# Kernel tuning notes

Measured on AMD Instinct MI355X. Metric: run time of the kernel, lower is better.

The kernel has to match this reference:

```python
import jax, jax.numpy as jnp
import numpy as np
import math

B, S, HID = 2, 2048, 2048
H, HKV, D, L = 16, 4, 128, 64
THETA = 10000.0
N_REP = H // HKV


def _rope(t, pos, theta=THETA):
    # t: [B, h, S, D], pos: [B, S] int
    d = t.shape[-1]
    inv_freq = 1.0 / (theta ** (jnp.arange(0, d, 2, dtype=jnp.float32) / d))  # [d/2]
    ang = pos.astype(jnp.float32)[:, :, None] * inv_freq  # [B, S, d/2]
    cos = jnp.concatenate([jnp.cos(ang), jnp.cos(ang)], axis=-1)[:, None]  # [B,1,S,d]
    sin = jnp.concatenate([jnp.sin(ang), jnp.sin(ang)], axis=-1)[:, None]
    t1, t2 = t[..., : d // 2], t[..., d // 2 :]
    rot = jnp.concatenate([-t2, t1], axis=-1)
    return t * cos + rot * sin


def setup_inputs() -> dict:
    key = jax.random.key(0)
    ks = jax.random.split(key, 9)
    sc = lambda fin: 1.0 / math.sqrt(fin)
    x = jax.random.normal(ks[0], (B, S, HID), dtype=jnp.float32)
    position_ids = jnp.broadcast_to(jnp.arange(S, dtype=jnp.int32), (B, S))
    # additive causal mask [1,1,S,S]
    causal = jnp.triu(jnp.full((S, S), -1e9, dtype=jnp.float32), k=1)
    attention_mask = causal[None, None]
    Wq = jax.random.normal(ks[1], (HID, H * D), dtype=jnp.float32) * sc(HID)
    Wk = jax.random.normal(ks[2], (HID, HKV * D), dtype=jnp.float32) * sc(HID)
    Wv = jax.random.normal(ks[3], (HID, HKV * D), dtype=jnp.float32) * sc(HID)
    Wql = jax.random.normal(ks[4], (D, L), dtype=jnp.float32) * sc(D)
    Wkl = jax.random.normal(ks[5], (D, L), dtype=jnp.float32) * sc(D)
    Wvl = jax.random.normal(ks[6], (D, L), dtype=jnp.float32) * sc(D)
    Wo = jax.random.normal(ks[7], (H * D, HID), dtype=jnp.float32) * sc(H * D)
    return {"x": x, "position_ids": position_ids, "attention_mask": attention_mask,
            "Wq": Wq, "Wk": Wk, "Wv": Wv, "Wql": Wql, "Wkl": Wkl, "Wvl": Wvl, "Wo": Wo}


def reference(x, position_ids, attention_mask, Wq, Wk, Wv, Wql, Wkl, Wvl, Wo):
    b, s, _ = x.shape
    q = (x @ Wq).reshape(b, s, H, D).transpose(0, 2, 1, 3)    # [B,H,S,D]
    k = (x @ Wk).reshape(b, s, HKV, D).transpose(0, 2, 1, 3)  # [B,HKV,S,D]
    v = (x @ Wv).reshape(b, s, HKV, D).transpose(0, 2, 1, 3)
    q = _rope(q, position_ids)
    k = _rope(k, position_ids)
    # latent compression per head-dim
    q_l = jnp.einsum('bhsd,dl->bhsl', q, Wql)  # [B,H,S,L]
    k_l = jnp.einsum('bhsd,dl->bhsl', k, Wkl)  # [B,HKV,S,L]
    v_l = jnp.einsum('bhsd,dl->bhsl', v, Wvl)
    k_l = jnp.repeat(k_l, N_REP, axis=1)  # repeat_kv -> [B,H,S,L]
    v_l = jnp.repeat(v_l, N_REP, axis=1)
    scale = math.sqrt(L)
    attn = jnp.einsum('bhql,bhkl->bhqk', q_l, k_l) / scale
    attn = attn + attention_mask
    attn = jax.nn.softmax(attn, axis=-1)
    out = jnp.einsum('bhqk,bhkl->bhql', attn, v_l)  # [B,H,S,L]
    if L < D:
        out = jnp.pad(out, ((0, 0), (0, 0), (0, 0), (0, D - L)))
    out = out.transpose(0, 2, 1, 3).reshape(b, s, H * D)
    return out @ Wo
```

## Files before the change

### kernel.cpp

```cpp
#include <hip/hip_runtime.h>
#include <cstddef>

constexpr int kB   = 2;
constexpr int kS   = 2048;
constexpr int kHID = 2048;
constexpr int kH   = 16;
constexpr int kHKV = 4;
constexpr int kD   = 128;
constexpr int kL   = 64;
constexpr int kTok = kB * kS;
constexpr int kNQKV = kH * kD + 2 * kHKV * kD;

typedef __attribute__((ext_vector_type(8))) short bf16x8;
typedef __attribute__((ext_vector_type(4))) float f32x4;

static __device__ __forceinline__ short f2bf(float f) {
  union { float f; unsigned u; } v{f};
  const unsigned r = (v.u + 0x7fff + ((v.u >> 16) & 1)) >> 16;
  return (short)r;
}
static __device__ __forceinline__ float bf2f(short s) {
  union { unsigned u; float f; } v;
  v.u = ((unsigned)(unsigned short)s) << 16;
  return v.f;
}

static __device__ __forceinline__ bf16x8 pack8(float4 a, float4 b) {
  bf16x8 r;
  r[0] = f2bf(a.x); r[1] = f2bf(a.y); r[2] = f2bf(a.z); r[3] = f2bf(a.w);
  r[4] = f2bf(b.x); r[5] = f2bf(b.y); r[6] = f2bf(b.z); r[7] = f2bf(b.w);
  return r;
}

static __device__ __forceinline__ unsigned cvt_pk_bf16(float lo, float hi) {
  unsigned r;
  asm("v_cvt_pk_bf16_f32 %0, %1, %2" : "=v"(r) : "v"(lo), "v"(hi));
  return r;
}

typedef __attribute__((address_space(3))) void       lds_void;
typedef __attribute__((address_space(1))) const void gm_void;
static __device__ __forceinline__ void gload16(const void* g, void* l) {
  __builtin_amdgcn_global_load_lds((gm_void*)g, (lds_void*)l, 16, 0, 0);
}

static __device__ __forceinline__ int2 xcd_swz(int nx, int ny) {
  int wg = blockIdx.y * nx + blockIdx.x;
  const int cpx = (nx * ny) >> 3;
  wg = (wg & 7) * cpx + (wg >> 3);
  int2 r; r.x = wg % nx; r.y = wg / nx;
  return r;
}

__global__ __launch_bounds__(256) void prep_all(
    const float* __restrict__ x, const int* __restrict__ pos,
    const float* __restrict__ Wq, const float* __restrict__ Wk,
    const float* __restrict__ Wv, const float* __restrict__ Wo,
    const float* __restrict__ Wql, const float* __restrict__ Wkl,
    const float* __restrict__ Wvl, short* __restrict__ x_bf,
    float* __restrict__ tbl, short* __restrict__ Wqkv,
    short* __restrict__ WoT, short* __restrict__ WqlT,
    short* __restrict__ WklT, short* __restrict__ WvlT) {
  __shared__ float T[64][65];
  const int bidg = blockIdx.x;
  const int tid = threadIdx.x;

  if (bidg < 4096) {
    const int i = bidg * 256 + tid;
    const float4 a = *(const float4*)&x[(size_t)i * 8];
    const float4 b = *(const float4*)&x[(size_t)i * 8 + 4];
    *(bf16x8*)&x_bf[(size_t)i * 8] = pack8(a, b);
    return;
  }
  if (bidg < 5120) {
    const int idx = (bidg - 4096) * 256 + tid;
    const int i = idx & 63, t = idx >> 6;
    const float p = (float)pos[t];
    const float inv_freq = expf(-(float)i * (9.210340371976184f / 64.0f));
    const float ang = p * inv_freq;
    tbl[t * 128 + i]      = cosf(ang);
    tbl[t * 128 + 64 + i] = sinf(ang);
    return;
  }
  const int rr = tid >> 4, cc = tid & 15;
  if (bidg < 6656) {
    const int idx = bidg - 5120;
    const int n0 = (idx % 48) * 64, k0 = (idx / 48) * 64;
    const float* in; int Nin, nl0;
    if (n0 < 2048)      { in = Wq; Nin = 2048; nl0 = n0; }
    else if (n0 < 2560) { in = Wk; Nin = 512;  nl0 = n0 - 2048; }
    else                { in = Wv; Nin = 512;  nl0 = n0 - 2560; }
#pragma unroll
    for (int ii = 0; ii < 4; ++ii) {
      const int kr = rr + ii * 16;
      const float4 v = *(const float4*)&in[(size_t)(k0 + kr) * Nin + nl0 + cc * 4];
      T[kr][cc * 4 + 0] = v.x; T[kr][cc * 4 + 1] = v.y;
      T[kr][cc * 4 + 2] = v.z; T[kr][cc * 4 + 3] = v.w;
    }
    __syncthreads();
#pragma unroll
    for (int ii = 0; ii < 4; ++ii) {
      const int n = rr + ii * 16;
      const short4 s4 = make_short4(f2bf(T[cc*4+0][n]), f2bf(T[cc*4+1][n]),
                                    f2bf(T[cc*4+2][n]), f2bf(T[cc*4+3][n]));
      *(short4*)&Wqkv[(size_t)(n0 + n) * kHID + k0 + cc * 4] = s4;
    }
    return;
  }
  if (bidg < 7168) {
    const int idx = bidg - 6656;
    const int n0 = (idx % 32) * 64, k0 = (idx / 32) * 64;
#pragma unroll
    for (int ii = 0; ii < 4; ++ii) {
      const int kr = rr + ii * 16;
      const int gr = (((k0 + kr) >> 6) << 7) + ((k0 + kr) & 63);
      const float4 v = *(const float4*)&Wo[(size_t)gr * kHID + n0 + cc * 4];
      T[kr][cc * 4 + 0] = v.x; T[kr][cc * 4 + 1] = v.y;
      T[kr][cc * 4 + 2] = v.z; T[kr][cc * 4 + 3] = v.w;
    }
    __syncthreads();
#pragma unroll
    for (int ii = 0; ii < 4; ++ii) {
      const int n = rr + ii * 16;
      const short4 s4 = make_short4(f2bf(T[cc*4+0][n]), f2bf(T[cc*4+1][n]),
                                    f2bf(T[cc*4+2][n]), f2bf(T[cc*4+3][n]));
      *(short4*)&WoT[(size_t)(n0 + n) * (kH * kL) + k0 + cc * 4] = s4;
    }
    return;
  }
  {
    const int idx = bidg - 7168;
    const int k0 = (idx & 1) * 64;
    const int z = idx >> 1;
    const float* in; short* out; float scale;
    if (z == 0)      { in = Wql; out = WqlT; scale = 0.125f; }
    else if (z == 1) { in = Wkl; out = WklT; scale = 1.0f; }
    else             { in = Wvl; out = WvlT; scale = 1.0f; }
#pragma unroll
    for (int ii = 0; ii < 4; ++ii) {
      const int kr = rr + ii * 16;
      const float4 v = *(const float4*)&in[(size_t)(k0 + kr) * kL + cc * 4];
      T[kr][cc * 4 + 0] = v.x * scale; T[kr][cc * 4 + 1] = v.y * scale;
      T[kr][cc * 4 + 2] = v.z * scale; T[kr][cc * 4 + 3] = v.w * scale;
    }
    __syncthreads();
#pragma unroll
    for (int ii = 0; ii < 4; ++ii) {
      const int n = rr + ii * 16;
      const short4 s4 = make_short4(f2bf(T[cc*4+0][n]), f2bf(T[cc*4+1][n]),
                                    f2bf(T[cc*4+2][n]), f2bf(T[cc*4+3][n]));
      *(short4*)&out[(size_t)n * kD + k0 + cc * 4] = s4;
    }
  }
}

__global__ __launch_bounds__(512) void gemm_qkv8(
    const short* __restrict__ A, const short* __restrict__ Bt,
    short* __restrict__ C0, short* __restrict__ C1, short* __restrict__ C2,
    int K) {
  __shared__ short As[2][256 * 64];
  __shared__ short Bs[2][256 * 64];
  const int tid = threadIdx.x;
  const int lane = tid & 63, w = tid >> 6;
  const int lr = lane & 15, lk = lane >> 4;
  const int wm = w >> 2, wn = w & 3;
  const int2 sw = xcd_swz(kNQKV / 256, kTok / 256);
  const int row0 = sw.y * 256, col0 = sw.x * 256;
  const int NT = K >> 6;

  auto stage = [&](int kt) {
    const int b = kt & 1;
    const int k0 = kt << 6;
#pragma unroll
    for (int j = 0; j < 4; ++j) {
      const int idx = j * 512 + tid;
      const int row = idx >> 3, blk = idx & 7;
      const int gcol = k0 + ((blk ^ (row & 7)) << 3);
      gload16(A + (size_t)(row0 + row) * K + gcol, &As[b][row * 64 + blk * 8]);
    }
#pragma unroll
    for (int j = 0; j < 4; ++j) {
      const int idx = j * 512 + tid;
      const int row = idx >> 3, blk = idx & 7;
      const int gcol = k0 + ((blk ^ (row & 7)) << 3);
      gload16(Bt + (size_t)(col0 + row) * K + gcol, &Bs[b][row * 64 + blk * 8]);
    }
  };

  f32x4 acc[8][4] = {};

  stage(0);
  for (int t = 0; t < NT; ++t) {
    const int b = t & 1;
    if (t + 1 < NT) {
      stage(t + 1);
      asm volatile("s_waitcnt vmcnt(8)" ::: "memory");
    } else {
      asm volatile("s_waitcnt vmcnt(0)" ::: "memory");
    }
    __builtin_amdgcn_s_barrier();

    bf16x8 bb[4][2];
#pragma unroll
    for (int n = 0; n < 4; ++n) {
      const int row = wn * 64 + n * 16 + lr;
#pragma unroll
      for (int ch = 0; ch < 2; ++ch) {
        const int blk = (ch * 4 + lk) ^ (row & 7);
        bb[n][ch] = *(const bf16x8*)&Bs[b][row * 64 + blk * 8];
      }
    }
#pragma unroll
    for (int qm = 0; qm < 2; ++qm) {
      bf16x8 a[4][2];
#pragma unroll
      for (int j = 0; j < 4; ++j) {
        const int row = wm * 128 + (qm * 4 + j) * 16 + lr;
#pragma unroll
        for (int ch = 0; ch < 2; ++ch) {
          const int blk = (ch * 4 + lk) ^ (row & 7);
          a[j][ch] = *(const bf16x8*)&As[b][row * 64 + blk * 8];
        }
      }
      __builtin_amdgcn_s_setprio(1);
#pragma unroll
      for (int j = 0; j < 4; ++j)
#pragma unroll
        for (int n = 0; n < 4; ++n)
#pragma unroll
          for (int ch = 0; ch < 2; ++ch)
            acc[qm * 4 + j][n] = __builtin_amdgcn_mfma_f32_16x16x32_bf16(
                a[j][ch], bb[n][ch], acc[qm * 4 + j][n], 0, 0, 0);
      __builtin_amdgcn_s_setprio(0);
    }
    __builtin_amdgcn_s_barrier();
  }

  short* dst; int ld, cb;
  if (col0 < 2048)      { dst = C0; ld = 2048; cb = col0; }
  else if (col0 < 2560) { dst = C1; ld = 512;  cb = col0 - 2048; }
  else                  { dst = C2; ld = 512;  cb = col0 - 2560; }
  const int crow0 = row0 + wm * 128 + lk * 4;
  const int ccol0 = cb + wn * 64 + lr;
#pragma unroll
  for (int mf = 0; mf < 8; ++mf)
#pragma unroll
    for (int nf = 0; nf < 4; ++nf)
#pragma unroll
      for (int r = 0; r < 4; ++r)
        dst[(size_t)(crow0 + mf * 16 + r) * ld + ccol0 + nf * 16] =
            f2bf(acc[mf][nf][r]);
}

__global__ __launch_bounds__(512) void gemm_out8(
    const short* __restrict__ A, const short* __restrict__ Bt,
    float* __restrict__ C, int M, int N, int K) {
  __shared__ short As[2][256 * 64];
  __shared__ short Bs[2][128 * 64];
  const int tid = threadIdx.x;
  const int lane = tid & 63, w = tid >> 6;
  const int lr = lane & 15, lk = lane >> 4;
  const int wm = w >> 2, wn = w & 3;
  const int2 sw = xcd_swz(N / 128, M / 256);
  const int row0 = sw.y * 256, col0 = sw.x * 128;
  const int NT = K >> 6;

  auto stage = [&](int kt) {
    const int b = kt & 1;
    const int k0 = kt << 6;
#pragma unroll
    for (int j = 0; j < 4; ++j) {
      const int idx = j * 512 + tid;
      const int row = idx >> 3, blk = idx & 7;
      const int gcol = k0 + ((blk ^ (row & 7)) << 3);
      gload16(A + (size_t)(row0 + row) * K + gcol, &As[b][row * 64 + blk * 8]);
    }
#pragma unroll
    for (int j = 0; j < 2; ++j) {
      const int idx = j * 512 + tid;
      const int row = idx >> 3, blk = idx & 7;
      const int gcol = k0 + ((blk ^ (row & 7)) << 3);
      gload16(Bt + (size_t)(col0 + row) * K + gcol, &Bs[b][row * 64 + blk * 8]);
    }
  };

  f32x4 acc[8][2] = {};

  stage(0);
  for (int t = 0; t < NT; ++t) {
    const int b = t & 1;
    if (t + 1 < NT) {
      stage(t + 1);
      asm volatile("s_waitcnt vmcnt(6)" ::: "memory");
    } else {
      asm volatile("s_waitcnt vmcnt(0)" ::: "memory");
    }
    __builtin_amdgcn_s_barrier();

    bf16x8 bb[2][2];
#pragma unroll
    for (int n = 0; n < 2; ++n) {
      const int row = wn * 32 + n * 16 + lr;
#pragma unroll
      for (int ch = 0; ch < 2; ++ch) {
        const int blk = (ch * 4 + lk) ^ (row & 7);
        bb[n][ch] = *(const bf16x8*)&Bs[b][row * 64 + blk * 8];
      }
    }
#pragma unroll
    for (int qm = 0; qm < 2; ++qm) {
      bf16x8 a[4][2];
#pragma unroll
      for (int j = 0; j < 4; ++j) {
        const int row = wm * 128 + (qm * 4 + j) * 16 + lr;
#pragma unroll
        for (int ch = 0; ch < 2; ++ch) {
          const int blk = (ch * 4 + lk) ^ (row & 7);
          a[j][ch] = *(const bf16x8*)&As[b][row * 64 + blk * 8];
        }
      }
      __builtin_amdgcn_s_setprio(1);
#pragma unroll
      for (int j = 0; j < 4; ++j)
#pragma unroll
        for (int n = 0; n < 2; ++n)
#pragma unroll
          for (int ch = 0; ch < 2; ++ch)
            acc[qm * 4 + j][n] = __builtin_amdgcn_mfma_f32_16x16x32_bf16(
                a[j][ch], bb[n][ch], acc[qm * 4 + j][n], 0, 0, 0);
      __builtin_amdgcn_s_setprio(0);
    }
    __builtin_amdgcn_s_barrier();
  }

  const int crow0 = row0 + wm * 128 + lk * 4;
  const int ccol0 = col0 + wn * 32 + lr;
#pragma unroll
  for (int mf = 0; mf < 8; ++mf)
#pragma unroll
    for (int nf = 0; nf < 2; ++nf)
#pragma unroll
      for (int r = 0; r < 4; ++r)
        C[(size_t)(crow0 + mf * 16 + r) * N + ccol0 + nf * 16] = acc[mf][nf][r];
}

__global__ __launch_bounds__(256) void rope_latent_all(
    const short* __restrict__ qb, const short* __restrict__ kb,
    const short* __restrict__ vb, const short* __restrict__ WqlT,
    const short* __restrict__ WklT, const short* __restrict__ WvlT,
    const float* __restrict__ tbl, short* __restrict__ q_l,
    short* __restrict__ k_l, short* __restrict__ v_lT) {
  __shared__ short Tw[4][1280];
  const int yz = blockIdx.y;
  const short* in; const short* WT; short* out; int nh; bool ROPE, TR;
  int bh;
  if (yz < 32)      { in = qb; WT = WqlT; out = q_l;  nh = kH;   ROPE = true;  TR = false; bh = yz; }
  else if (yz < 40) { in = kb; WT = WklT; out = k_l;  nh = kHKV; ROPE = true;  TR = false; bh = yz - 32; }
  else              { in = vb; WT = WvlT; out = v_lT; nh = kHKV; ROPE = false; TR = true;  bh = yz - 40; }

  const int tid = threadIdx.x;
  const int lane = tid & 63;
  const int w = tid >> 6;
  const int lr = lane & 15;
  const int lk = lane >> 4;
  const int b = bh / nh, h = bh % nh;
  const int s0 = blockIdx.x * 64;
  const int srow = s0 + w * 16 + lr;
  const int tok = b * kS + srow;

  const short* ip = in + ((size_t)tok * nh + h) * kD + lk * 8;
  bf16x8 raw[4];
#pragma unroll
  for (int ch = 0; ch < 4; ++ch) raw[ch] = *(const bf16x8*)(ip + ch * 32);

  bf16x8 af[4];
  if (ROPE) {
    float a[4][8];
#pragma unroll
    for (int ch = 0; ch < 4; ++ch)
#pragma unroll
      for (int i = 0; i < 8; ++i) a[ch][i] = bf2f(raw[ch][i]);
    const float* tb = tbl + (size_t)tok * 128;
    float c[2][8], sn[2][8];
#pragma unroll
    for (int g = 0; g < 2; ++g) {
      const float4 cA = *(const float4*)(tb + g * 32 + lk * 8);
      const float4 cB = *(const float4*)(tb + g * 32 + lk * 8 + 4);
      const float4 sA = *(const float4*)(tb + 64 + g * 32 + lk * 8);
      const float4 sB = *(const float4*)(tb + 64 + g * 32 + lk * 8 + 4);
      c[g][0] = cA.x; c[g][1] = cA.y; c[g][2] = cA.z; c[g][3] = cA.w;
      c[g][4] = cB.x; c[g][5] = cB.y; c[g][6] = cB.z; c[g][7] = cB.w;
      sn[g][0] = sA.x; sn[g][1] = sA.y; sn[g][2] = sA.z; sn[g][3] = sA.w;
      sn[g][4] = sB.x; sn[g][5] = sB.y; sn[g][6] = sB.z; sn[g][7] = sB.w;
    }
    float o[4][8];
#pragma unroll
    for (int g = 0; g < 2; ++g)
#pragma unroll
      for (int i = 0; i < 8; ++i) {
        o[g][i]     = a[g][i]     * c[g][i] - a[g + 2][i] * sn[g][i];
        o[g + 2][i] = a[g + 2][i] * c[g][i] + a[g][i]     * sn[g][i];
      }
#pragma unroll
    for (int ch = 0; ch < 4; ++ch)
#pragma unroll
      for (int i = 0; i < 8; ++i) af[ch][i] = f2bf(o[ch][i]);
  } else {
#pragma unroll
    for (int ch = 0; ch < 4; ++ch) af[ch] = raw[ch];
  }

  f32x4 acc[4] = {};
#pragma unroll
  for (int cb = 0; cb < 4; ++cb) {
#pragma unroll
    for (int ch = 0; ch < 4; ++ch) {
      const bf16x8 bfrag =
          *(const bf16x8*)&WT[(size_t)(cb * 16 + lr) * kD + ch * 32 + lk * 8];
      acc[cb] = __builtin_amdgcn_mfma_f32_16x16x32_bf16(af[ch], bfrag,
                                                        acc[cb], 0, 0, 0);
    }
  }

  short* T = Tw[w];
  if (!TR) {
#pragma unroll
    for (int cb = 0; cb < 4; ++cb)
#pragma unroll
      for (int r = 0; r < 4; ++r)
        T[(lk * 4 + r) * 72 + cb * 16 + lr] = f2bf(acc[cb][r]);
    asm volatile("s_waitcnt lgkmcnt(0)" ::: "memory");
#pragma unroll
    for (int it = 0; it < 2; ++it) {
      const int idx = it * 64 + lane;
      const int row = idx >> 3, c8 = (idx & 7) << 3;
      *(bf16x8*)&out[((size_t)bh * kS + s0 + w * 16 + row) * kL + c8] =
          *(const bf16x8*)&T[row * 72 + c8];
    }
  } else {
#pragma unroll
    for (int cb = 0; cb < 4; ++cb)
#pragma unroll
      for (int r = 0; r < 4; ++r)
        T[(cb * 16 + lr) * 20 + lk * 4 + r] = f2bf(acc[cb][r]);
    asm volatile("s_waitcnt lgkmcnt(0)" ::: "memory");
    const size_t orow = ((size_t)bh * kL + lane) * kS + s0 + w * 16;
#pragma unroll
    for (int c = 0; c < 4; ++c)
      *(short4*)&out[orow + c * 4] = *(const short4*)&T[lane * 20 + c * 4];
  }
}

__global__ __launch_bounds__(512) void flash_attn_mfma(
    const short* __restrict__ ql, const short* __restrict__ kl,
    const short* __restrict__ vlT, short* __restrict__ attn_out) {
  constexpr int LDK = 72;
  constexpr int LDV = 136;
  __shared__ short Kt[2][128 * LDK];
  __shared__ short Vt[2][64 * LDV];

  const int tid = threadIdx.x;
  const int lane = tid & 63;
  const int w = tid >> 6;
  const int lr = lane & 15;
  const int lk = lane >> 4;
  const int bid = blockIdx.y;
  const int bx = (bid < 8) ? (2 * bid) : (31 - 2 * bid);
  const int q0 = bx * 128;
  const int bh = blockIdx.x;
  const int b = bh >> 4, h = bh & 15;
  const int hk = h >> 2;
  const int wrow = q0 + w * 16;

  const short* qrow = ql + ((size_t)bh * kS + wrow + lr) * kL;
  bf16x8 qf[2];
  qf[0] = *(const bf16x8*)(qrow + lk * 8);
  qf[1] = *(const bf16x8*)(qrow + 32 + lk * 8);

  f32x4 Of[4] = {};
  float m = -3.0e38f, l = 0.f;

  const short* kgp = kl + (size_t)(b * kHKV + hk) * kS * kL;
  const short* vgp = vlT + (size_t)(b * kHKV + hk) * kL * kS;
  const int ntiles = bx + 1;

  const int kr0 = tid >> 3,          kc0 = (tid & 7) << 3;
  const int kr1 = (512 + tid) >> 3,  kc1 = (tid & 7) << 3;
  const int vr0 = tid >> 4,          vc0 = (tid & 15) << 3;
  const int vr1 = (512 + tid) >> 4,  vc1 = (tid & 15) << 3;

  *(bf16x8*)&Kt[0][kr0 * LDK + kc0] = *(const bf16x8*)(kgp + (size_t)kr0 * kL + kc0);
  *(bf16x8*)&Kt[0][kr1 * LDK + kc1] = *(const bf16x8*)(kgp + (size_t)kr1 * kL + kc1);
  *(bf16x8*)&Vt[0][vr0 * LDV + vc0] = *(const bf16x8*)(vgp + (size_t)vr0 * kS + vc0);
  *(bf16x8*)&Vt[0][vr1 * LDV + vc1] = *(const bf16x8*)(vgp + (size_t)vr1 * kS + vc1);
  __syncthreads();

  const int sl0 = lr + ((lane & 16) << 1);
  const bool hisel = (lk >> 1) != 0;

  int cur = 0;
  for (int t = 0; t < ntiles; ++t) {
    const int j0 = t * 128;
    const bool pre = (t + 1 < ntiles);
    bf16x8 krn0, krn1, vrn0, vrn1;
    if (pre) {
      const int jn = j0 + 128;
      krn0 = *(const bf16x8*)(kgp + (size_t)(jn + kr0) * kL + kc0);
      krn1 = *(const bf16x8*)(kgp + (size_t)(jn + kr1) * kL + kc1);
      vrn0 = *(const bf16x8*)(vgp + (size_t)vr0 * kS + jn + vc0);
      vrn1 = *(const bf16x8*)(vgp + (size_t)vr1 * kS + jn + vc1);
    }

    const short* Kc = &Kt[cur][0];
    const short* Vc = &Vt[cur][0];
#pragma unroll
    for (int sub = 0; sub < 2; ++sub) {
      const int js = j0 + sub * 64;
      if (js > wrow) continue;

      f32x4 Sf[4];
      __builtin_amdgcn_s_setprio(1);
#pragma unroll
      for (int cb = 0; cb < 4; ++cb) {
        f32x4 acc = {};
#pragma unroll
        for (int ch = 0; ch < 2; ++ch) {
          const bf16x8 kf = *(const bf16x8*)
              &Kc[(sub * 64 + cb * 16 + lr) * LDK + ch * 32 + lk * 8];
          acc = __builtin_amdgcn_mfma_f32_16x16x32_bf16(kf, qf[ch], acc, 0, 0, 0);
        }
        Sf[cb] = acc;
      }
      __builtin_amdgcn_s_setprio(0);

      float mt = -3.0e38f;
      if (js + 63 > wrow) {
#pragma unroll
        for (int cb = 0; cb < 4; ++cb)
#pragma unroll
          for (int r = 0; r < 4; ++r) {
            float s = Sf[cb][r];
            if ((js + cb * 16 + lk * 4 + r) > (wrow + lr)) s = -3.0e38f;
            Sf[cb][r] = s;
            mt = fmaxf(mt, s);
          }
      } else {
#pragma unroll
        for (int cb = 0; cb < 4; ++cb)
#pragma unroll
          for (int r = 0; r < 4; ++r) mt = fmaxf(mt, Sf[cb][r]);
      }
      mt = fmaxf(mt, __shfl_xor(mt, 16));
      mt = fmaxf(mt, __shfl_xor(mt, 32));

      const bool resc = __any((int)(mt > m + 8.f));
      if (resc) {
        const float mnew = fmaxf(m, mt);
        const float corr = __expf(m - mnew);
        m = mnew;
        l *= corr;
#pragma unroll
        for (int lb = 0; lb < 4; ++lb)
#pragma unroll
          for (int r = 0; r < 4; ++r) Of[lb][r] *= corr;
      }

      unsigned pk[4][2];
#pragma unroll
      for (int cb = 0; cb < 4; ++cb) {
        const float p0 = __expf(Sf[cb][0] - m);
        const float p1 = __expf(Sf[cb][1] - m);
        const float p2 = __expf(Sf[cb][2] - m);
        const float p3 = __expf(Sf[cb][3] - m);
        l += (p0 + p1) + (p2 + p3);
        pk[cb][0] = cvt_pk_bf16(p0, p1);
        pk[cb][1] = cvt_pk_bf16(p2, p3);
      }

#pragma unroll
      for (int ch = 0; ch < 2; ++ch) {
        const unsigned lo00 = __shfl(pk[2 * ch][0], sl0);
        const unsigned lo01 = __shfl(pk[2 * ch][1], sl0);
        const unsigned lo10 = __shfl(pk[2 * ch][0], sl0 + 16);
        const unsigned lo11 = __shfl(pk[2 * ch][1], sl0 + 16);
        const unsigned hi00 = __shfl(pk[2 * ch + 1][0], sl0);
        const unsigned hi01 = __shfl(pk[2 * ch + 1][1], sl0);
        const unsigned hi10 = __shfl(pk[2 * ch + 1][0], sl0 + 16);
        const unsigned hi11 = __shfl(pk[2 * ch + 1][1], sl0 + 16);
        union { unsigned u[4]; bf16x8 v; } pf;
        pf.u[0] = hisel ? hi00 : lo00;
        pf.u[1] = hisel ? hi01 : lo01;
        pf.u[2] = hisel ? hi10 : lo10;
        pf.u[3] = hisel ? hi11 : lo11;
        __builtin_amdgcn_s_setprio(1);
#pragma unroll
        for (int lb = 0; lb < 4; ++lb) {
          const bf16x8 vf = *(const bf16x8*)
              &Vc[(lb * 16 + lr) * LDV + sub * 64 + ch * 32 + lk * 8];
          Of[lb] = __builtin_amdgcn_mfma_f32_16x16x32_bf16(vf, pf.v, Of[lb], 0, 0, 0);
        }
        __builtin_amdgcn_s_setprio(0);
      }
    }

    if (pre) {
      *(bf16x8*)&Kt[cur ^ 1][kr0 * LDK + kc0] = krn0;
      *(bf16x8*)&Kt[cur ^ 1][kr1 * LDK + kc1] = krn1;
      *(bf16x8*)&Vt[cur ^ 1][vr0 * LDV + vc0] = vrn0;
      *(bf16x8*)&Vt[cur ^ 1][vr1 * LDV + vc1] = vrn1;
    }
    __syncthreads();
    cur ^= 1;
  }

  l += __shfl_xor(l, 16);
  l += __shfl_xor(l, 32);
  const float inv = 1.f / l;
  const size_t rowoff =
      (size_t)(b * kS + wrow + lr) * (kH * kL) + h * kL + lk * 4;
#pragma unroll
  for (int lb = 0; lb < 4; ++lb) {
    const short4 s4 = make_short4(f2bf(Of[lb][0] * inv), f2bf(Of[lb][1] * inv),
                                  f2bf(Of[lb][2] * inv), f2bf(Of[lb][3] * inv));
    *(short4*)&attn_out[rowoff + lb * 16] = s4;
  }
}

extern "C" void kernel_launch(void* const* d_in, const int* in_sizes, int n_in,
                              void* d_out, int out_size, void* d_ws, size_t ws_size,
                              hipStream_t stream) {
  const float* x    = (const float*)d_in[0];
  const int*   pos  = (const int*)d_in[1];
  const float* Wq   = (const float*)d_in[3];
  const float* Wk   = (const float*)d_in[4];
  const float* Wv   = (const float*)d_in[5];
  const float* Wql  = (const float*)d_in[6];
  const float* Wkl  = (const float*)d_in[7];
  const float* Wvl  = (const float*)d_in[8];
  const float* Wo   = (const float*)d_in[9];
  float* out = (float*)d_out;

  char* p = (char*)d_ws;
  short* x_bf  = (short*)p; p += (size_t)kTok * kHID * 2;
  short* Wqkv  = (short*)p; p += (size_t)kNQKV * kHID * 2;
  short* WoT   = (short*)p; p += (size_t)kHID * (kH * kL) * 2;
  short* WqlT  = (short*)p; p += (size_t)kL * kD * 2;
  short* WklT  = (short*)p; p += (size_t)kL * kD * 2;
  short* WvlT  = (short*)p; p += (size_t)kL * kD * 2;
  float* tbl   = (float*)p; p += (size_t)kTok * 128 * 4;
  short* k_buf = (short*)p; p += (size_t)kTok * kHKV * kD * 2;
  short* v_buf = (short*)p; p += (size_t)kTok * kHKV * kD * 2;
  short* q_l   = (short*)p; p += (size_t)kB * kH * kS * kL * 2;
  short* k_l   = (short*)p; p += (size_t)kB * kHKV * kS * kL * 2;
  short* v_lT  = (short*)p; p += (size_t)kB * kHKV * kS * kL * 2;
  short* attn  = (short*)p;
  short* q_buf = (short*)d_out;

  prep_all<<<7174, 256, 0, stream>>>(x, pos, Wq, Wk, Wv, Wo, Wql, Wkl, Wvl,
                                     x_bf, tbl, Wqkv, WoT, WqlT, WklT, WvlT);

  gemm_qkv8<<<dim3(kNQKV / 256, kTok / 256), 512, 0, stream>>>(
      x_bf, Wqkv, q_buf, k_buf, v_buf, kHID);

  rope_latent_all<<<dim3(kS / 64, 48), 256, 0, stream>>>(
      q_buf, k_buf, v_buf, WqlT, WklT, WvlT, tbl, q_l, k_l, v_lT);

  flash_attn_mfma<<<dim3(kB * kH, kS / 128), 512, 0, stream>>>(
      q_l, k_l, v_lT, attn);

  gemm_out8<<<dim3(kHID / 128, kTok / 256), 512, 0, stream>>>(
      attn, WoT, out, kTok, kHID, kH * kL);
}
```

Before: 180.5 us.

## Pair complementary causal query tiles per block to share K/V loads

Each flash-attention block now handles two query tiles, bxA and 15-bxA, so every block does the same amount of causal work. Each K/V tile is staged in shared memory once and reused by both query sets, and the grid is halved. The aim is to cut redundant K/V global loads and remove load imbalance across blocks. In exchange each thread holds twice the register state (two Q fragments, two O accumulators, two sets of softmax stats), which may lower occupancy, and there are half as many blocks to fill the GPU.

```diff
diff --git a/kernel.cpp b/kernel.cpp
--- a/kernel.cpp
+++ b/kernel.cpp
@@ -464,25 +464,27 @@
   const int w = tid >> 6;
   const int lr = lane & 15;
   const int lk = lane >> 4;
-  const int bid = blockIdx.y;
-  const int bx = (bid < 8) ? (2 * bid) : (31 - 2 * bid);
-  const int q0 = bx * 128;
+  const int bxA = blockIdx.y;
+  const int bxB = 15 - bxA;
   const int bh = blockIdx.x;
   const int b = bh >> 4, h = bh & 15;
   const int hk = h >> 2;
-  const int wrow = q0 + w * 16;
-
-  const short* qrow = ql + ((size_t)bh * kS + wrow + lr) * kL;
-  bf16x8 qf[2];
-  qf[0] = *(const bf16x8*)(qrow + lk * 8);
-  qf[1] = *(const bf16x8*)(qrow + 32 + lk * 8);
-
-  f32x4 Of[4] = {};
-  float m = -3.0e38f, l = 0.f;
+  const int wrowA = bxA * 128 + w * 16;
+  const int wrowB = bxB * 128 + w * 16;
+
+  const short* qbase = ql + (size_t)bh * kS * kL;
+  bf16x8 qfA[2], qfB[2];
+  qfA[0] = *(const bf16x8*)(qbase + (size_t)(wrowA + lr) * kL + lk * 8);
+  qfA[1] = *(const bf16x8*)(qbase + (size_t)(wrowA + lr) * kL + 32 + lk * 8);
+  qfB[0] = *(const bf16x8*)(qbase + (size_t)(wrowB + lr) * kL + lk * 8);
+  qfB[1] = *(const bf16x8*)(qbase + (size_t)(wrowB + lr) * kL + 32 + lk * 8);
+
+  f32x4 OfA[4] = {}, OfB[4] = {};
+  float mA = -3.0e38f, lA = 0.f, mB = -3.0e38f, lB = 0.f;
 
   const short* kgp = kl + (size_t)(b * kHKV + hk) * kS * kL;
   const short* vgp = vlT + (size_t)(b * kHKV + hk) * kL * kS;
-  const int ntiles = bx + 1;
+  const int ntiles = bxB + 1;
 
   const int kr0 = tid >> 3,          kc0 = (tid & 7) << 3;
   const int kr1 = (512 + tid) >> 3,  kc1 = (tid & 7) << 3;
@@ -497,6 +499,93 @@
 
   const int sl0 = lr + ((lane & 16) << 1);
   const bool hisel = (lk >> 1) != 0;
+
+  auto proc = [&](const bf16x8 (&qf)[2], f32x4 (&Of)[4], float& m, float& l,
+                  int wrow, int js, int sub, const short* Kc, const short* Vc) {
+    f32x4 Sf[4];
+    __builtin_amdgcn_s_setprio(1);
+#pragma unroll
+    for (int cb = 0; cb < 4; ++cb) {
+      f32x4 acc = {};
+#pragma unroll
+      for (int ch = 0; ch < 2; ++ch) {
+        const bf16x8 kf = *(const bf16x8*)
+            &Kc[(sub * 64 + cb * 16 + lr) * LDK + ch * 32 + lk * 8];
+        acc = __builtin_amdgcn_mfma_f32_16x16x32_bf16(kf, qf[ch], acc, 0, 0, 0);
+      }
+      Sf[cb] = acc;
+    }
+    __builtin_amdgcn_s_setprio(0);
+
+    float mt = -3.0e38f;
+    if (js + 63 > wrow) {
+#pragma unroll
+      for (int cb = 0; cb < 4; ++cb)
+#pragma unroll
+        for (int r = 0; r < 4; ++r) {
+          float s = Sf[cb][r];
+          if ((js + cb * 16 + lk * 4 + r) > (wrow + lr)) s = -3.0e38f;
+          Sf[cb][r] = s;
+          mt = fmaxf(mt, s);
+        }
+    } else {
+#pragma unroll
+      for (int cb = 0; cb < 4; ++cb)
+#pragma unroll
+        for (int r = 0; r < 4; ++r) mt = fmaxf(mt, Sf[cb][r]);
+    }
+    mt = fmaxf(mt, __shfl_xor(mt, 16));
+    mt = fmaxf(mt, __shfl_xor(mt, 32));
+
+    const bool resc = __any((int)(mt > m + 8.f));
+    if (resc) {
+      const float mnew = fmaxf(m, mt);
+      const float corr = __expf(m - mnew);
+      m = mnew;
+      l *= corr;
+#pragma unroll
+      for (int lb = 0; lb < 4; ++lb)
+#pragma unroll
+        for (int r = 0; r < 4; ++r) Of[lb][r] *= corr;
+    }
+
+    unsigned pk[4][2];
+#pragma unroll
+    for (int cb = 0; cb < 4; ++cb) {
+      const float p0 = __expf(Sf[cb][0] - m);
+      const float p1 = __expf(Sf[cb][1] - m);
+      const float p2 = __expf(Sf[cb][2] - m);
+      const float p3 = __expf(Sf[cb][3] - m);
+      l += (p0 + p1) + (p2 + p3);
+      pk[cb][0] = cvt_pk_bf16(p0, p1);
+      pk[cb][1] = cvt_pk_bf16(p2, p3);
+    }
+
+#pragma unroll
+    for (int ch = 0; ch < 2; ++ch) {
+      const unsigned lo00 = __shfl(pk[2 * ch][0], sl0);
+      const unsigned lo01 = __shfl(pk[2 * ch][1], sl0);
+      const unsigned lo10 = __shfl(pk[2 * ch][0], sl0 + 16);
+      const unsigned lo11 = __shfl(pk[2 * ch][1], sl0 + 16);
+      const unsigned hi00 = __shfl(pk[2 * ch + 1][0], sl0);
+      const unsigned hi01 = __shfl(pk[2 * ch + 1][1], sl0);
+      const unsigned hi10 = __shfl(pk[2 * ch + 1][0], sl0 + 16);
+      const unsigned hi11 = __shfl(pk[2 * ch + 1][1], sl0 + 16);
+      union { unsigned u[4]; bf16x8 v; } pf;
+      pf.u[0] = hisel ? hi00 : lo00;
+      pf.u[1] = hisel ? hi01 : lo01;
+      pf.u[2] = hisel ? hi10 : lo10;
+      pf.u[3] = hisel ? hi11 : lo11;
+      __builtin_amdgcn_s_setprio(1);
+#pragma unroll
+      for (int lb = 0; lb < 4; ++lb) {
+        const bf16x8 vf = *(const bf16x8*)
+            &Vc[(lb * 16 + lr) * LDV + sub * 64 + ch * 32 + lk * 8];
+        Of[lb] = __builtin_amdgcn_mfma_f32_16x16x32_bf16(vf, pf.v, Of[lb], 0, 0, 0);
+      }
+      __builtin_amdgcn_s_setprio(0);
+    }
+  };
 
   int cur = 0;
   for (int t = 0; t < ntiles; ++t) {
@@ -516,91 +605,8 @@
 #pragma unroll
     for (int sub = 0; sub < 2; ++sub) {
       const int js = j0 + sub * 64;
-      if (js > wrow) continue;
-
-      f32x4 Sf[4];
-      __builtin_amdgcn_s_setprio(1);
-#pragma unroll
-      for (int cb = 0; cb < 4; ++cb) {
-        f32x4 acc = {};
-#pragma unroll
-        for (int ch = 0; ch < 2; ++ch) {
-          const bf16x8 kf = *(const bf16x8*)
-              &Kc[(sub * 64 + cb * 16 + lr) * LDK + ch * 32 + lk * 8];
-          acc = __builtin_amdgcn_mfma_f32_16x16x32_bf16(kf, qf[ch], acc, 0, 0, 0);
-        }
-        Sf[cb] = acc;
-      }
-      __builtin_amdgcn_s_setprio(0);
-
-      float mt = -3.0e38f;
-      if (js + 63 > wrow) {
-#pragma unroll
-        for (int cb = 0; cb < 4; ++cb)
-#pragma unroll
-          for (int r = 0; r < 4; ++r) {
-            float s = Sf[cb][r];
-            if ((js + cb * 16 + lk * 4 + r) > (wrow + lr)) s = -3.0e38f;
-            Sf[cb][r] = s;
-            mt = fmaxf(mt, s);
-          }
-      } else {
-#pragma unroll
-        for (int cb = 0; cb < 4; ++cb)
-#pragma unroll
-          for (int r = 0; r < 4; ++r) mt = fmaxf(mt, Sf[cb][r]);
-      }
-      mt = fmaxf(mt, __shfl_xor(mt, 16));
-      mt = fmaxf(mt, __shfl_xor(mt, 32));
-
-      const bool resc = __any((int)(mt > m + 8.f));
-      if (resc) {
-        const float mnew = fmaxf(m, mt);
-        const float corr = __expf(m - mnew);
-        m = mnew;
-        l *= corr;
-#pragma unroll
-        for (int lb = 0; lb < 4; ++lb)
-#pragma unroll
-          for (int r = 0; r < 4; ++r) Of[lb][r] *= corr;
-      }
-
-      unsigned pk[4][2];
-#pragma unroll
-      for (int cb = 0; cb < 4; ++cb) {
-        const float p0 = __expf(Sf[cb][0] - m);
-        const float p1 = __expf(Sf[cb][1] - m);
-        const float p2 = __expf(Sf[cb][2] - m);
-        const float p3 = __expf(Sf[cb][3] - m);
-        l += (p0 + p1) + (p2 + p3);
-        pk[cb][0] = cvt_pk_bf16(p0, p1);
-        pk[cb][1] = cvt_pk_bf16(p2, p3);
-      }
-
-#pragma unroll
-      for (int ch = 0; ch < 2; ++ch) {
-        const unsigned lo00 = __shfl(pk[2 * ch][0], sl0);
-        const unsigned lo01 = __shfl(pk[2 * ch][1], sl0);
-        const unsigned lo10 = __shfl(pk[2 * ch][0], sl0 + 16);
-        const unsigned lo11 = __shfl(pk[2 * ch][1], sl0 + 16);
-        const unsigned hi00 = __shfl(pk[2 * ch + 1][0], sl0);
-        const unsigned hi01 = __shfl(pk[2 * ch + 1][1], sl0);
-        const unsigned hi10 = __shfl(pk[2 * ch + 1][0], sl0 + 16);
-        const unsigned hi11 = __shfl(pk[2 * ch + 1][1], sl0 + 16);
-        union { unsigned u[4]; bf16x8 v; } pf;
-        pf.u[0] = hisel ? hi00 : lo00;
-        pf.u[1] = hisel ? hi01 : lo01;
-        pf.u[2] = hisel ? hi10 : lo10;
-        pf.u[3] = hisel ? hi11 : lo11;
-        __builtin_amdgcn_s_setprio(1);
-#pragma unroll
-        for (int lb = 0; lb < 4; ++lb) {
-          const bf16x8 vf = *(const bf16x8*)
-              &Vc[(lb * 16 + lr) * LDV + sub * 64 + ch * 32 + lk * 8];
-          Of[lb] = __builtin_amdgcn_mfma_f32_16x16x32_bf16(vf, pf.v, Of[lb], 0, 0, 0);
-        }
-        __builtin_amdgcn_s_setprio(0);
-      }
+      if (js <= wrowA) proc(qfA, OfA, mA, lA, wrowA, js, sub, Kc, Vc);
+      if (js <= wrowB) proc(qfB, OfB, mB, lB, wrowB, js, sub, Kc, Vc);
     }
 
     if (pre) {
@@ -613,16 +619,21 @@
     cur ^= 1;
   }
 
-  l += __shfl_xor(l, 16);
-  l += __shfl_xor(l, 32);
-  const float inv = 1.f / l;
-  const size_t rowoff =
-      (size_t)(b * kS + wrow + lr) * (kH * kL) + h * kL + lk * 4;
+  lA += __shfl_xor(lA, 16);  lA += __shfl_xor(lA, 32);
+  lB += __shfl_xor(lB, 16);  lB += __shfl_xor(lB, 32);
+  const float invA = 1.f / lA, invB = 1.f / lB;
+  const size_t rowA =
+      (size_t)(b * kS + wrowA + lr) * (kH * kL) + h * kL + lk * 4;
+  const size_t rowB =
+      (size_t)(b * kS + wrowB + lr) * (kH * kL) + h * kL + lk * 4;
 #pragma unroll
   for (int lb = 0; lb < 4; ++lb) {
-    const short4 s4 = make_short4(f2bf(Of[lb][0] * inv), f2bf(Of[lb][1] * inv),
-                                  f2bf(Of[lb][2] * inv), f2bf(Of[lb][3] * inv));
-    *(short4*)&attn_out[rowoff + lb * 16] = s4;
+    const short4 sA = make_short4(f2bf(OfA[lb][0] * invA), f2bf(OfA[lb][1] * invA),
+                                  f2bf(OfA[lb][2] * invA), f2bf(OfA[lb][3] * invA));
+    *(short4*)&attn_out[rowA + lb * 16] = sA;
+    const short4 sB = make_short4(f2bf(OfB[lb][0] * invB), f2bf(OfB[lb][1] * invB),
+                                  f2bf(OfB[lb][2] * invB), f2bf(OfB[lb][3] * invB));
+    *(short4*)&attn_out[rowB + lb * 16] = sB;
   }
 }
 
@@ -665,7 +676,7 @@
   rope_latent_all<<<dim3(kS / 64, 48), 256, 0, stream>>>(
       q_buf, k_buf, v_buf, WqlT, WklT, WvlT, tbl, q_l, k_l, v_lT);
 
-  flash_attn_mfma<<<dim3(kB * kH, kS / 128), 512, 0, stream>>>(
+  flash_attn_mfma<<<dim3(kB * kH, 8), 512, 0, stream>>>(
       q_l, k_l, v_lT, attn);
 
   gemm_out8<<<dim3(kHID / 128, kTok / 256), 512, 0, stream>>>(
```

Result: no change. 183.3 us (+1.5%).
